# Kernel tuning notes

Measured on AMD Instinct MI355X. Metric: run time of the kernel, lower is better.

Reference implementation:

```python
import jax, jax.numpy as jnp
from jax import lax
import numpy as np

B, TE, TD, C, H, L, V, BLOCK = 2, 1024, 1024, 512, 8, 4, 32000, 1024
HD = C // H  # 64


def setup_inputs() -> dict:
    key = jax.random.key(0)
    ks = iter(jax.random.split(key, 64))
    def w(*shape):
        return jax.random.normal(next(ks), shape, jnp.float32) * 0.02
    d = {}
    d["enc_inp"] = jax.random.randint(next(ks), (B, TE), 0, V, dtype=jnp.int32)
    d["dec_inp"] = jax.random.randint(next(ks), (B, TD), 0, V, dtype=jnp.int32)
    d["enc_inp_mask"] = jnp.ones((B, TE), jnp.int32)
    d["tok_emb"] = w(V, C)
    d["pos_emb"] = w(BLOCK, C)
    for p in ["e", "d_sa", "d_ca"]:
        d[p + "_wq"] = w(L, H, C, HD)
        d[p + "_wk"] = w(L, H, C, HD)
        d[p + "_wv"] = w(L, H, C, HD)
        d[p + "_wo"] = w(L, C, C)
        d[p + "_bo"] = jnp.zeros((L, C), jnp.float32)
    for n in ["e_ln1", "e_ln2", "d_ln1", "d_ln2", "d_ln3"]:
        d[n + "_g"] = jnp.ones((L, C), jnp.float32)
        d[n + "_b"] = jnp.zeros((L, C), jnp.float32)
    for p in ["e", "d"]:
        d[p + "_w1"] = w(L, C, 4 * C)
        d[p + "_b1"] = jnp.zeros((L, 4 * C), jnp.float32)
        d[p + "_w2"] = w(L, 4 * C, C)
        d[p + "_b2"] = jnp.zeros((L, C), jnp.float32)
    d["out_w"] = w(C, V)
    d["out_b"] = jnp.zeros((V,), jnp.float32)
    return d


def _ln(x, g, b):
    m = jnp.mean(x, -1, keepdims=True)
    v = jnp.mean((x - m) ** 2, -1, keepdims=True)
    return (x - m) / jnp.sqrt(v + 1e-5) * g + b


def _mha(x, kv, wq, wk, wv, wo, bo, mask, causal):
    # x: [B,T,C], kv: [B,S,C], wq/wk/wv: [H,C,HD]
    q = jnp.einsum('btc,hcd->bhtd', x, wq)
    k = jnp.einsum('bsc,hcd->bhsd', kv, wk)
    v = jnp.einsum('bsc,hcd->bhsd', kv, wv)
    s = jnp.einsum('bhtd,bhsd->bhts', q, k) * (HD ** -0.5)
    if causal:
        T, S = s.shape[-2], s.shape[-1]
        s = jnp.where(jnp.tril(jnp.ones((T, S), bool)), s, -jnp.inf)
    if mask is not None:
        s = jnp.where(mask[:, None, None, :] != 0, s, -jnp.inf)
    a = jax.nn.softmax(s, axis=-1)
    o = jnp.einsum('bhts,bhsd->bthd', a, v).reshape(x.shape[0], x.shape[1], -1)
    return o @ wo + bo


def reference(enc_inp, dec_inp, enc_inp_mask, tok_emb, pos_emb,
              e_wq, e_wk, e_wv, e_wo, e_bo,
              d_sa_wq, d_sa_wk, d_sa_wv, d_sa_wo, d_sa_bo,
              d_ca_wq, d_ca_wk, d_ca_wv, d_ca_wo, d_ca_bo,
              e_ln1_g, e_ln1_b, e_ln2_g, e_ln2_b,
              d_ln1_g, d_ln1_b, d_ln2_g, d_ln2_b, d_ln3_g, d_ln3_b,
              e_w1, e_b1, e_w2, e_b2, d_w1, d_b1, d_w2, d_b2,
              out_w, out_b):
    enc = tok_emb[enc_inp] + pos_emb[:enc_inp.shape[1]]
    dec = tok_emb[dec_inp] + pos_emb[:dec_inp.shape[1]]

    def enc_step(x, p):
        ln1g, ln1b, wq, wk, wv, wo, bo, ln2g, ln2b, w1, b1, w2, b2 = p
        h = _ln(x, ln1g, ln1b)
        x = x + _mha(h, h, wq, wk, wv, wo, bo, enc_inp_mask, False)
        h = _ln(x, ln2g, ln2b)
        x = x + jnp.maximum(h @ w1 + b1, 0.0) @ w2 + b2
        return x, None

    enc_out, _ = lax.scan(enc_step, enc, (e_ln1_g, e_ln1_b, e_wq, e_wk, e_wv, e_wo, e_bo,
                                          e_ln2_g, e_ln2_b, e_w1, e_b1, e_w2, e_b2))

    def dec_step(x, p):
        (ln1g, ln1b, sawq, sawk, sawv, sawo, sabo,
         ln2g, ln2b, cawq, cawk, cawv, cawo, cabo,
         ln3g, ln3b, w1, b1, w2, b2) = p
        h = _ln(x, ln1g, ln1b)
        x = x + _mha(h, h, sawq, sawk, sawv, sawo, sabo, None, True)
        # torch code applies the same cross-attn LayerNorm to both x and encoder_output
        hq = _ln(x, ln2g, ln2b)
        hk = _ln(enc_out, ln2g, ln2b)
        x = x + _mha(hq, hk, cawq, cawk, cawv, cawo, cabo, enc_inp_mask, False)
        h = _ln(x, ln3g, ln3b)
        x = x + jnp.maximum(h @ w1 + b1, 0.0) @ w2 + b2
        return x, None

    dec_out, _ = lax.scan(dec_step, dec, (d_ln1_g, d_ln1_b, d_sa_wq, d_sa_wk, d_sa_wv, d_sa_wo, d_sa_bo,
                                          d_ln2_g, d_ln2_b, d_ca_wq, d_ca_wk, d_ca_wv, d_ca_wo, d_ca_bo,
                                          d_ln3_g, d_ln3_b, d_w1, d_b1, d_w2, d_b2))

    logits = dec_out @ out_w + out_b  # [B, T_dec, V]
    return logits
```

## Files before the change

### kernel.cpp

```cpp
#include <hip/hip_runtime.h>
#include <hip/hip_bf16.h>
#include <math.h>

#define Cdim 512
#define Hn   8
#define HDim 64
#define Ld   4
#define Tn   1024
#define Bn   2
#define NTOK 2048
#define FF   2048
#define Vn   32000

typedef __bf16 bf16_t;
typedef __bf16 bf16x8 __attribute__((ext_vector_type(8)));
typedef __bf16 bf16x4 __attribute__((ext_vector_type(4)));
typedef float  f32x4  __attribute__((ext_vector_type(4)));

__device__ __forceinline__ void ln_wave(const float* __restrict__ xr,
    const float* __restrict__ g, const float* __restrict__ bb,
    bf16_t* __restrict__ yr, int lane)
{
    f32x4 a = *(const f32x4*)&xr[lane * 8];
    f32x4 c = *(const f32x4*)&xr[lane * 8 + 4];
    float s = a[0] + a[1] + a[2] + a[3] + c[0] + c[1] + c[2] + c[3];
    #pragma unroll
    for (int o = 1; o < 64; o <<= 1) s += __shfl_xor(s, o, 64);
    float mean = s * (1.f / Cdim);
    float d[8], qv = 0.f;
    #pragma unroll
    for (int k = 0; k < 4; k++) { d[k] = a[k] - mean; d[4 + k] = c[k] - mean; }
    #pragma unroll
    for (int k = 0; k < 8; k++) qv += d[k] * d[k];
    #pragma unroll
    for (int o = 1; o < 64; o <<= 1) qv += __shfl_xor(qv, o, 64);
    float inv = rsqrtf(qv * (1.f / Cdim) + 1e-5f);
    f32x4 g0 = *(const f32x4*)&g[lane * 8],  g1 = *(const f32x4*)&g[lane * 8 + 4];
    f32x4 b0 = *(const f32x4*)&bb[lane * 8], b1 = *(const f32x4*)&bb[lane * 8 + 4];
    bf16x8 o;
    #pragma unroll
    for (int k = 0; k < 4; k++) {
        o[k]     = (bf16_t)(d[k]     * inv * g0[k] + b0[k]);
        o[4 + k] = (bf16_t)(d[4 + k] * inv * g1[k] + b1[k]);
    }
    *(bf16x8*)&yr[lane * 8] = o;
}

__global__ __launch_bounds__(256) void ln_k(const float* __restrict__ x,
    const float* __restrict__ g, const float* __restrict__ bb, bf16_t* __restrict__ y)
{
    int wid = threadIdx.x >> 6, lane = threadIdx.x & 63;
    int row = blockIdx.x * 4 + wid;
    ln_wave(x + (long)row * Cdim, g, bb, y + (long)row * Cdim, lane);
}

__global__ __launch_bounds__(256) void ln2_k(const float* __restrict__ x1,
    const float* __restrict__ x2, const float* __restrict__ g,
    const float* __restrict__ bb, bf16_t* __restrict__ y1, bf16_t* __restrict__ y2)
{
    int wid = threadIdx.x >> 6, lane = threadIdx.x & 63;
    int row = blockIdx.x * 4 + wid;
    const float* x = (row < NTOK) ? x1 : x2;
    bf16_t*      y = (row < NTOK) ? y1 : y2;
    int r = row & (NTOK - 1);
    ln_wave(x + (long)r * Cdim, g, bb, y + (long)r * Cdim, lane);
}

__global__ __launch_bounds__(256) void embed_ln_k(const int* __restrict__ inp,
    const float* __restrict__ tok, const float* __restrict__ pos,
    const float* __restrict__ g, const float* __restrict__ bb,
    float* __restrict__ x, bf16_t* __restrict__ y)
{
    int wid = threadIdx.x >> 6, lane = threadIdx.x & 63;
    int bt = blockIdx.x * 4 + wid;
    int t = bt & (Tn - 1);
    long toff = (long)inp[bt] * Cdim;
    f32x4 a = *(const f32x4*)&tok[toff + lane * 8];
    f32x4 c = *(const f32x4*)&tok[toff + lane * 8 + 4];
    f32x4 pa = *(const f32x4*)&pos[(long)t * Cdim + lane * 8];
    f32x4 pc = *(const f32x4*)&pos[(long)t * Cdim + lane * 8 + 4];
    a += pa; c += pc;
    float* xr = x + (long)bt * Cdim;
    *(f32x4*)&xr[lane * 8] = a;
    *(f32x4*)&xr[lane * 8 + 4] = c;
    float s = a[0] + a[1] + a[2] + a[3] + c[0] + c[1] + c[2] + c[3];
    #pragma unroll
    for (int o = 1; o < 64; o <<= 1) s += __shfl_xor(s, o, 64);
    float mean = s * (1.f / Cdim);
    float d[8], qv = 0.f;
    #pragma unroll
    for (int k = 0; k < 4; k++) { d[k] = a[k] - mean; d[4 + k] = c[k] - mean; }
    #pragma unroll
    for (int k = 0; k < 8; k++) qv += d[k] * d[k];
    #pragma unroll
    for (int o = 1; o < 64; o <<= 1) qv += __shfl_xor(qv, o, 64);
    float inv = rsqrtf(qv * (1.f / Cdim) + 1e-5f);
    f32x4 g0 = *(const f32x4*)&g[lane * 8],  g1 = *(const f32x4*)&g[lane * 8 + 4];
    f32x4 b0 = *(const f32x4*)&bb[lane * 8], b1 = *(const f32x4*)&bb[lane * 8 + 4];
    bf16x8 o;
    #pragma unroll
    for (int k = 0; k < 4; k++) {
        o[k]     = (bf16_t)(d[k]     * inv * g0[k] + b0[k]);
        o[4 + k] = (bf16_t)(d[4 + k] * inv * g1[k] + b1[k]);
    }
    *(bf16x8*)&y[(long)bt * Cdim + lane * 8] = o;
}

struct Ptr3 { const float* p[3]; };
__global__ __launch_bounds__(256) void tcvt_b_k(Ptr3 srcs, bf16_t* __restrict__ dst,
    int R, int Cc, int lps, long dstStride)
{
    int z = blockIdx.z; int s = z / lps, l = z - s * lps;
    const float* in = srcs.p[s] + (long)l * R * Cc;
    bf16_t* op = dst + (long)z * dstStride;
    __shared__ float t[64][65];
    int r0 = blockIdx.y * 64, c0 = blockIdx.x * 64;
    int tx = threadIdx.x & 63, ty = threadIdx.x >> 6;
    #pragma unroll
    for (int i = 0; i < 16; i++)
        t[ty + i * 4][tx] = in[(long)(r0 + ty + i * 4) * Cc + c0 + tx];
    __syncthreads();
    #pragma unroll
    for (int i = 0; i < 16; i++) {
        int cc = ty + i * 4;
        op[(long)(c0 + cc) * R + r0 + tx] = (bf16_t)t[tx][cc];
    }
}

struct QkvSrc { const float* p[9]; };
__global__ __launch_bounds__(256) void tcvt_qkv_k(QkvSrc srcs, bf16_t* __restrict__ outp)
{
    int z = blockIdx.z;
    int si = z >> 5, zb = (z >> 3) & 3, zh = z & 7;
    int set = si / 3, part = si - set * 3;
    const float* in = srcs.p[si] + (long)zb * (Hn * Cdim * HDim) + (long)zh * (Cdim * HDim);
    bf16_t* op = outp + ((long)set * Ld + zb) * (1536L * Cdim)
                      + (long)part * 512 * Cdim + (long)zh * 64 * Cdim;
    __shared__ float t[64][65];
    int r0 = blockIdx.y * 64;
    int tx = threadIdx.x & 63, ty = threadIdx.x >> 6;
    #pragma unroll
    for (int i = 0; i < 16; i++)
        t[ty + i * 4][tx] = in[(long)(r0 + ty + i * 4) * HDim + tx];
    __syncthreads();
    #pragma unroll
    for (int i = 0; i < 16; i++) {
        int cc = ty + i * 4;
        op[(long)cc * Cdim + r0 + tx] = (bf16_t)t[tx][cc];
    }
}

template<int BM, int BN, int BK, bool BIAS, bool RELU, bool RES, bool OBF,
         bool VOUT, int SWZM, bool XOUT, bool COAL>
__global__ __launch_bounds__(256) void mgemm_k(
    const bf16_t* __restrict__ A, const bf16_t* __restrict__ A2, int aSplit,
    const bf16_t* __restrict__ Bt, const float* __restrict__ bias,
    const float* __restrict__ res, void* __restrict__ Cout,
    bf16_t* __restrict__ xout, bf16_t* __restrict__ vtout, int vSplit,
    int K, int lda, int ldb, int ldc)
{
    constexpr int MR = BM / 32;
    constexpr int NR = BN / 32;
    constexpr int KK = BK / 32;
    constexpr int LPR = BK / 8;
    __shared__ bf16_t As0[BM * BK];
    __shared__ bf16_t As1[BM * BK];
    __shared__ bf16_t Bs0[BN * BK];
    __shared__ bf16_t Bs1[BN * BK];
    __shared__ float cws[COAL ? 4 * 16 * 36 : 1];

    int tid = threadIdx.x;
    int wv = tid >> 6, lane = tid & 63;
    int bm, bn;
    if constexpr (SWZM > 0) {
        int lin = blockIdx.y * gridDim.x + blockIdx.x;
        int tot = gridDim.x * gridDim.y;
        int chunk = tot >> 3;
        int e = (lin & 7) * chunk + (lin >> 3);
        bm = (e % SWZM) * BM;
        bn = (e / SWZM) * BN;
    } else {
        bm = blockIdx.y * BM; bn = blockIdx.x * BN;
    }
    const bf16_t* Ab = (bn < aSplit) ? A : A2;
    int wr = wv >> 1, wc = wv & 1;

    f32x4 acc[MR][NR];
    #pragma unroll
    for (int i = 0; i < MR; i++)
        #pragma unroll
        for (int j = 0; j < NR; j++)
            acc[i][j] = (f32x4){0.f, 0.f, 0.f, 0.f};

    constexpr int RPW = 512 / BK;
    constexpr int RPP = 2048 / BK;
    const int sr  = lane / LPR;
    const int sc8 = ((lane % LPR) ^ (sr & (LPR - 1))) * 8;
    const int r16 = lane & 15, g4 = lane >> 4;

    auto stage = [&](int k0, bf16_t (&Asb)[BM * BK], bf16_t (&Bsb)[BN * BK]) {
        #pragma unroll
        for (int p = 0; p < BM * BK / 2048; p++) {
            int rb = p * RPP + wv * RPW;
            const bf16_t* g = Ab + (long)(bm + rb + sr) * lda + (k0 + sc8);
            __builtin_amdgcn_global_load_lds(
                (const __attribute__((address_space(1))) void*)g,
                (__attribute__((address_space(3))) void*)&Asb[rb * BK],
                16, 0, 0);
        }
        #pragma unroll
        for (int p = 0; p < BN * BK / 2048; p++) {
            int rb = p * RPP + wv * RPW;
            const bf16_t* g = Bt + (long)(bn + rb + sr) * ldb + (k0 + sc8);
            __builtin_amdgcn_global_load_lds(
                (const __attribute__((address_space(1))) void*)g,
                (__attribute__((address_space(3))) void*)&Bsb[rb * BK],
                16, 0, 0);
        }
    };
    auto compute = [&](bf16_t (&Asb)[BM * BK], bf16_t (&Bsb)[BN * BK]) {
        #pragma unroll
        for (int kk = 0; kk < KK; kk++) {
            bf16x8 bkk[NR];
            #pragma unroll
            for (int j = 0; j < NR; j++) {
                int row = wc * (BN / 2) + j * 16 + r16;
                bkk[j] = *(const bf16x8*)&Bsb[row * BK + (((kk * 4 + g4) ^ (row & (LPR - 1))) * 8)];
            }
            #pragma unroll
            for (int i = 0; i < MR; i++) {
                int row = wr * (BM / 2) + i * 16 + r16;
                bf16x8 a = *(const bf16x8*)&Asb[row * BK + (((kk * 4 + g4) ^ (row & (LPR - 1))) * 8)];
                #pragma unroll
                for (int j = 0; j < NR; j++)
                    acc[i][j] = __builtin_amdgcn_mfma_f32_16x16x32_bf16(a, bkk[j], acc[i][j], 0, 0, 0);
            }
        }
    };

    int nIt = K / BK;
    stage(0, As0, Bs0);
    for (int it = 0; it < nIt; it += 2) {
        __syncthreads();
        if (it + 1 < nIt) stage((it + 1) * BK, As1, Bs1);
        compute(As0, Bs0);
        __syncthreads();
        if (it + 2 < nIt) stage((it + 2) * BK, As0, Bs0);
        if (it + 1 < nIt) compute(As1, Bs1);
    }

    if constexpr (COAL) {
        #pragma unroll
        for (int i = 0; i < MR; i++) {
            int gr0 = bm + wr * (BM / 2) + i * 16;
            #pragma unroll
            for (int hh = 0; hh < NR / 2; hh++) {
                #pragma unroll
                for (int jj = 0; jj < 2; jj++) {
                    int j = hh * 2 + jj;
                    int gc = bn + wc * (BN / 2) + j * 16 + r16;
                    float bv = BIAS ? bias[gc] : 0.f;
                    #pragma unroll
                    for (int q = 0; q < 4; q++) {
                        float v = acc[i][j][q];
                        if (BIAS) v += bv;
                        if (RELU) v = fmaxf(v, 0.f);
                        cws[(wv * 16 + g4 * 4 + q) * 36 + jj * 16 + r16] = v;
                    }
                }
                int gcb = bn + wc * (BN / 2) + hh * 32;
                if constexpr (OBF) {
                    int row = lane >> 2, c8 = (lane & 3) * 8;
                    f32x4 v0 = *(f32x4*)&cws[(wv * 16 + row) * 36 + c8];
                    f32x4 v1 = *(f32x4*)&cws[(wv * 16 + row) * 36 + c8 + 4];
                    long oidx = (long)(gr0 + row) * ldc + gcb + c8;
                    bf16x8 o;
                    #pragma unroll
                    for (int k = 0; k < 4; k++) { o[k] = (bf16_t)v0[k]; o[4 + k] = (bf16_t)v1[k]; }
                    *(bf16x8*)&((bf16_t*)Cout)[oidx] = o;
                } else {
                    #pragma unroll
                    for (int ps = 0; ps < 2; ps++) {
                        int row = (lane >> 3) + 8 * ps, c4 = (lane & 7) * 4;
                        f32x4 v = *(f32x4*)&cws[(wv * 16 + row) * 36 + c4];
                        long oidx = (long)(gr0 + row) * ldc + gcb + c4;
                        if (RES) v += *(const f32x4*)&res[oidx];
                        *(f32x4*)&((float*)Cout)[oidx] = v;
                        if (XOUT) {
                            bf16x4 o;
                            #pragma unroll
                            for (int k = 0; k < 4; k++) o[k] = (bf16_t)v[k];
                            *(bf16x4*)&xout[oidx] = o;
                        }
                    }
                }
            }
        }
    } else {
        #pragma unroll
        for (int i = 0; i < MR; i++) {
            #pragma unroll
            for (int j = 0; j < NR; j++) {
                int gr = bm + wr * (BM / 2) + i * 16 + g4 * 4;
                int gc = bn + wc * (BN / 2) + j * 16 + r16;
                float bv = BIAS ? bias[gc] : 0.f;
                #pragma unroll
                for (int q = 0; q < 4; q++) {
                    float v = acc[i][j][q];
                    if (BIAS) v += bv;
                    if (RELU) v = fmaxf(v, 0.f);
                    if (VOUT && gc >= vSplit) {
                        int row = gr + q;
                        int b = row >> 10, t = row & (Tn - 1);
                        vtout[((long)b * 512 + (gc - vSplit)) * Tn + t] = (bf16_t)v;
                    } else {
                        long oidx = (long)(gr + q) * ldc + gc;
                        if (RES)  v += res[oidx];
                        if (OBF) ((bf16_t*)Cout)[oidx] = (bf16_t)v;
                        else     ((float*) Cout)[oidx] = v;
                        if (XOUT) xout[oidx] = (bf16_t)v;
                    }
                }
            }
        }
    }
}

template<bool CAUSAL, bool HASMASK>
__global__ __launch_bounds__(512, 2) void flash_k(
    const bf16_t* __restrict__ qkv, const bf16_t* __restrict__ vt,
    const int* __restrict__ mask, bf16_t* __restrict__ ao)
{
    __shared__ bf16_t Kl[2][2][64][72];
    __shared__ bf16_t Vl[2][2][64][72];
    __shared__ bf16_t Pl[8][16][72];

    int qt = blockIdx.x, bh = blockIdx.y;
    int b = bh >> 3, h = bh & 7;
    int tid = threadIdx.x, wv = tid >> 6, lane = tid & 63;
    int wg = wv >> 2, wq4 = wv & 3;
    int r16 = lane & 15, g4 = lane >> 4;
    int gtid = tid & 255;

    const bf16_t* qb = qkv + ((long)(b * Tn + qt * 64 + wq4 * 16 + r16)) * 1536 + h * 64;
    bf16x8 aq0 = *(const bf16x8*)&qb[g4 * 8];
    bf16x8 aq1 = *(const bf16x8*)&qb[32 + g4 * 8];

    f32x4 acc[4];
    #pragma unroll
    for (int j = 0; j < 4; j++) acc[j] = (f32x4){0.f, 0.f, 0.f, 0.f};
    float m_[4], l_[4];
    #pragma unroll
    for (int q = 0; q < 4; q++) { m_[q] = -1e30f; l_[q] = 0.f; }

    int lastT = CAUSAL ? qt : (Tn / 64 - 1);
    int niter = CAUSAL ? (qt / 2 + 1) : (Tn / 128);
    int krow = gtid >> 3, kcol = (gtid & 7) * 8;

    bf16x8 kr[2], vr[2];
    int mv = 0;
    {
        int t0 = wg;
        if (t0 <= lastT) {
            int s0 = t0 * 64;
            #pragma unroll
            for (int i = 0; i < 2; i++)
                kr[i] = *(const bf16x8*)&qkv[((long)(b * Tn + s0 + krow + i * 32)) * 1536 + 512 + h * 64 + kcol];
            #pragma unroll
            for (int i = 0; i < 2; i++)
                vr[i] = *(const bf16x8*)&vt[((long)(bh * 64 + krow + i * 32)) * Tn + s0 + kcol];
            if (HASMASK) mv = mask[b * Tn + s0 + lane];
        }
    }

    for (int it = 0; it < niter; it++) {
        int cur = it & 1;
        int t = 2 * it + wg;
        bool active = t <= lastT;
        if (active) {
            #pragma unroll
            for (int i = 0; i < 2; i++) *(bf16x8*)&Kl[cur][wg][krow + i * 32][kcol] = kr[i];
            #pragma unroll
            for (int i = 0; i < 2; i++) *(bf16x8*)&Vl[cur][wg][krow + i * 32][kcol] = vr[i];
        }
        int mv_use = mv;
        __syncthreads();
        int tn = t + 2;
        if (it + 1 < niter && tn <= lastT) {
            int sn = tn * 64;
            #pragma unroll
            for (int i = 0; i < 2; i++)
                kr[i] = *(const bf16x8*)&qkv[((long)(b * Tn + sn + krow + i * 32)) * 1536 + 512 + h * 64 + kcol];
            #pragma unroll
            for (int i = 0; i < 2; i++)
                vr[i] = *(const bf16x8*)&vt[((long)(bh * 64 + krow + i * 32)) * Tn + sn + kcol];
            if (HASMASK) mv = mask[b * Tn + sn + lane];
        }
        if (!active) continue;

        f32x4 scv[4];
        __builtin_amdgcn_s_setprio(1);
        #pragma unroll
        for (int j = 0; j < 4; j++) {
            scv[j] = (f32x4){0.f, 0.f, 0.f, 0.f};
            bf16x8 bk0 = *(const bf16x8*)&Kl[cur][wg][j * 16 + r16][g4 * 8];
            bf16x8 bk1 = *(const bf16x8*)&Kl[cur][wg][j * 16 + r16][32 + g4 * 8];
            scv[j] = __builtin_amdgcn_mfma_f32_16x16x32_bf16(aq0, bk0, scv[j], 0, 0, 0);
            scv[j] = __builtin_amdgcn_mfma_f32_16x16x32_bf16(aq1, bk1, scv[j], 0, 0, 0);
        }
        __builtin_amdgcn_s_setprio(0);

        bool diag = CAUSAL && (t == qt);
        #pragma unroll
        for (int j = 0; j < 4; j++) {
            int col = j * 16 + r16;
            int mm = 1;
            if (HASMASK) mm = __shfl(mv_use, col, 64);
            #pragma unroll
            for (int q = 0; q < 4; q++) {
                float v = scv[j][q] * 0.125f;
                if (diag && col > wq4 * 16 + g4 * 4 + q) v = -1e30f;
                if (HASMASK && mm == 0) v = -1e30f;
                scv[j][q] = v;
            }
        }

        float pmax[4];
        #pragma unroll
        for (int q = 0; q < 4; q++) {
            float v = fmaxf(fmaxf(scv[0][q], scv[1][q]), fmaxf(scv[2][q], scv[3][q]));
            v = fmaxf(v, __shfl_xor(v, 1, 64));
            v = fmaxf(v, __shfl_xor(v, 2, 64));
            v = fmaxf(v, __shfl_xor(v, 4, 64));
            v = fmaxf(v, __shfl_xor(v, 8, 64));
            pmax[q] = v;
        }
        bool skip = __all(pmax[0] <= m_[0] + 8.f && pmax[1] <= m_[1] + 8.f &&
                          pmax[2] <= m_[2] + 8.f && pmax[3] <= m_[3] + 8.f);
        if (!skip) {
            #pragma unroll
            for (int q = 0; q < 4; q++) {
                float mnew = fmaxf(m_[q], pmax[q]);
                float rf = __expf(m_[q] - mnew);
                l_[q] *= rf;
                #pragma unroll
                for (int j = 0; j < 4; j++) acc[j][q] *= rf;
                m_[q] = mnew;
            }
        }
        #pragma unroll
        for (int q = 0; q < 4; q++) {
            float rs = 0.f;
            #pragma unroll
            for (int j = 0; j < 4; j++) {
                float pv = __expf(scv[j][q] - m_[q]);
                scv[j][q] = pv;
                rs += pv;
            }
            rs += __shfl_xor(rs, 1, 64);
            rs += __shfl_xor(rs, 2, 64);
            rs += __shfl_xor(rs, 4, 64);
            rs += __shfl_xor(rs, 8, 64);
            l_[q] += rs;
        }

        #pragma unroll
        for (int j = 0; j < 4; j++)
            #pragma unroll
            for (int q = 0; q < 4; q++)
                Pl[wv][g4 * 4 + q][j * 16 + r16] = (bf16_t)scv[j][q];
        asm volatile("s_waitcnt lgkmcnt(0)" ::: "memory");
        __builtin_amdgcn_sched_barrier(0);

        __builtin_amdgcn_s_setprio(1);
        #pragma unroll
        for (int c = 0; c < 2; c++) {
            bf16x8 pa = *(const bf16x8*)&Pl[wv][r16][c * 32 + g4 * 8];
            #pragma unroll
            for (int j = 0; j < 4; j++) {
                bf16x8 bv = *(const bf16x8*)&Vl[cur][wg][j * 16 + r16][c * 32 + g4 * 8];
                acc[j] = __builtin_amdgcn_mfma_f32_16x16x32_bf16(pa, bv, acc[j], 0, 0, 0);
            }
        }
        __builtin_amdgcn_s_setprio(0);
    }

    float* accS = (float*)&Kl[0][0][0][0];
    float* mlS  = accS + 64 * 64;
    __syncthreads();
    if (wg == 1) {
        #pragma unroll
        for (int j = 0; j < 4; j++)
            #pragma unroll
            for (int q = 0; q < 4; q++)
                accS[(wq4 * 16 + g4 * 4 + q) * 64 + j * 16 + r16] = acc[j][q];
        if (r16 == 0)
            #pragma unroll
            for (int q = 0; q < 4; q++) {
                mlS[(wq4 * 16 + g4 * 4 + q) * 2 + 0] = m_[q];
                mlS[(wq4 * 16 + g4 * 4 + q) * 2 + 1] = l_[q];
            }
    }
    __syncthreads();
    if (wg == 0) {
        bf16_t* aob = ao + ((long)(b * Tn + qt * 64 + wq4 * 16 + g4 * 4)) * Cdim + h * 64;
        #pragma unroll
        for (int q = 0; q < 4; q++) {
            int row = wq4 * 16 + g4 * 4 + q;
            float mB = mlS[row * 2], lB = mlS[row * 2 + 1];
            float mS = fmaxf(m_[q], mB);
            float fA = __expf(m_[q] - mS), fB = __expf(mB - mS);
            float lS = l_[q] * fA + lB * fB;
            float inv = 1.f / lS;
            #pragma unroll
            for (int j = 0; j < 4; j++) {
                float o = (acc[j][q] * fA + accS[row * 64 + j * 16 + r16] * fB) * inv;
                aob[(long)q * Cdim + j * 16 + r16] = (bf16_t)o;
            }
        }
    }
}

static void run_attn(hipStream_t stream, const bf16_t* hq, const bf16_t* hkv,
    const bf16_t* wqkv, const float* bo, const bf16_t* wo_t,
    float* xres, const int* mask, bool causal,
    bf16_t* qkv, bf16_t* vt, bf16_t* ao)
{
    dim3 blk(256);
    mgemm_k<64,128,64,false,false,false,true,true,0,false,false><<<dim3(12, 32, 1), blk, 0, stream>>>(
        hq, hkv, 512, wqkv, nullptr, nullptr, qkv, nullptr, vt, 1024,
        Cdim, Cdim, Cdim, 1536);
    if (causal)
        flash_k<true,false><<<dim3(Tn / 64, Bn * Hn), dim3(512), 0, stream>>>(qkv, vt, nullptr, ao);
    else
        flash_k<false,true><<<dim3(Tn / 64, Bn * Hn), dim3(512), 0, stream>>>(qkv, vt, mask, ao);
    mgemm_k<64,64,64,true,false,true,false,false,0,false,true><<<dim3(8, 32, 1), blk, 0, stream>>>(
        ao, ao, 1 << 30, wo_t, bo, xres, xres, nullptr, nullptr, 1 << 30,
        Cdim, Cdim, Cdim, Cdim);
}

extern "C" void kernel_launch(void* const* d_in, const int* in_sizes, int n_in,
                              void* d_out, int out_size, void* d_ws, size_t ws_size,
                              hipStream_t stream)
{
    (void)in_sizes; (void)n_in; (void)out_size; (void)ws_size;
    const int*   enc_inp  = (const int*)d_in[0];
    const int*   dec_inp  = (const int*)d_in[1];
    const int*   enc_mask = (const int*)d_in[2];
    const float* tok_emb  = (const float*)d_in[3];
    const float* pos_emb  = (const float*)d_in[4];
    const float* e_wq  = (const float*)d_in[5];
    const float* e_wk  = (const float*)d_in[6];
    const float* e_wv  = (const float*)d_in[7];
    const float* e_wo  = (const float*)d_in[8];
    const float* e_bo  = (const float*)d_in[9];
    const float* dsa_wq = (const float*)d_in[10];
    const float* dsa_wk = (const float*)d_in[11];
    const float* dsa_wv = (const float*)d_in[12];
    const float* dsa_wo = (const float*)d_in[13];
    const float* dsa_bo = (const float*)d_in[14];
    const float* dca_wq = (const float*)d_in[15];
    const float* dca_wk = (const float*)d_in[16];
    const float* dca_wv = (const float*)d_in[17];
    const float* dca_wo = (const float*)d_in[18];
    const float* dca_bo = (const float*)d_in[19];
    const float* e_ln1_g = (const float*)d_in[20];
    const float* e_ln1_b = (const float*)d_in[21];
    const float* e_ln2_g = (const float*)d_in[22];
    const float* e_ln2_b = (const float*)d_in[23];
    const float* d_ln1_g = (const float*)d_in[24];
    const float* d_ln1_b = (const float*)d_in[25];
    const float* d_ln2_g = (const float*)d_in[26];
    const float* d_ln2_b = (const float*)d_in[27];
    const float* d_ln3_g = (const float*)d_in[28];
    const float* d_ln3_b = (const float*)d_in[29];
    const float* e_w1 = (const float*)d_in[30];
    const float* e_b1 = (const float*)d_in[31];
    const float* e_w2 = (const float*)d_in[32];
    const float* e_b2 = (const float*)d_in[33];
    const float* d_w1 = (const float*)d_in[34];
    const float* d_b1 = (const float*)d_in[35];
    const float* d_w2 = (const float*)d_in[36];
    const float* d_b2 = (const float*)d_in[37];
    const float* out_w = (const float*)d_in[38];
    const float* out_b = (const float*)d_in[39];
    float* out = (float*)d_out;

    char* p = (char*)d_ws;
    auto takeB = [&](size_t bytes) { char* r = p; p += (bytes + 255) & ~(size_t)255; return r; };
    float*  x_enc = (float*)takeB(1048576ull * 4);
    float*  x_dec = (float*)takeB(1048576ull * 4);
    bf16_t* h     = (bf16_t*)takeB(1048576ull * 2);
    bf16_t* hk    = (bf16_t*)takeB(1048576ull * 2);
    bf16_t* qkv   = (bf16_t*)takeB(3145728ull * 2);
    bf16_t* vt    = (bf16_t*)takeB(1048576ull * 2);
    bf16_t* ao    = (bf16_t*)takeB(1048576ull * 2);
    bf16_t* xdb   = (bf16_t*)takeB(1048576ull * 2);
    bf16_t* mid   = (bf16_t*)takeB(4194304ull * 2);
    bf16_t* wqkv_t = (bf16_t*)takeB(12ull * 786432 * 2);
    bf16_t* wo_t   = (bf16_t*)takeB(12ull * 262144 * 2);
    bf16_t* w1_t   = (bf16_t*)takeB(8ull * 1048576 * 2);
    bf16_t* w2_t   = (bf16_t*)takeB(8ull * 1048576 * 2);
    bf16_t* outw_t = (bf16_t*)takeB(16384000ull * 2);

    dim3 blk(256);
    const long LQKV = 1536L * Cdim;

    QkvSrc qs;
    qs.p[0] = e_wq;   qs.p[1] = e_wk;   qs.p[2] = e_wv;
    qs.p[3] = dsa_wq; qs.p[4] = dsa_wk; qs.p[5] = dsa_wv;
    qs.p[6] = dca_wq; qs.p[7] = dca_wk; qs.p[8] = dca_wv;
    tcvt_qkv_k<<<dim3(1, 8, 288), blk, 0, stream>>>(qs, wqkv_t);
    Ptr3 pw;
    pw.p[0] = e_wo; pw.p[1] = dsa_wo; pw.p[2] = dca_wo;
    tcvt_b_k<<<dim3(8, 8, 12), blk, 0, stream>>>(pw, wo_t, Cdim, Cdim, 4, (long)Cdim * Cdim);
    pw.p[0] = e_w1; pw.p[1] = d_w1; pw.p[2] = nullptr;
    tcvt_b_k<<<dim3(32, 8, 8), blk, 0, stream>>>(pw, w1_t, Cdim, FF, 4, (long)Cdim * FF);
    pw.p[0] = e_w2; pw.p[1] = d_w2; pw.p[2] = nullptr;
    tcvt_b_k<<<dim3(8, 32, 8), blk, 0, stream>>>(pw, w2_t, FF, Cdim, 4, (long)FF * Cdim);
    pw.p[0] = out_w; pw.p[1] = nullptr; pw.p[2] = nullptr;
    tcvt_b_k<<<dim3(500, 8, 1), blk, 0, stream>>>(pw, outw_t, Cdim, Vn, 1, 0);

    embed_ln_k<<<NTOK / 4, blk, 0, stream>>>(enc_inp, tok_emb, pos_emb, e_ln1_g, e_ln1_b, x_enc, h);
    for (int l = 0; l < Ld; l++) {
        if (l) ln_k<<<NTOK / 4, blk, 0, stream>>>(x_enc, e_ln1_g + l * Cdim, e_ln1_b + l * Cdim, h);
        run_attn(stream, h, h,
                 wqkv_t + (long)l * LQKV, e_bo + l * Cdim, wo_t + (long)l * Cdim * Cdim,
                 x_enc, enc_mask, false, qkv, vt, ao);
        ln_k<<<NTOK / 4, blk, 0, stream>>>(x_enc, e_ln2_g + l * Cdim, e_ln2_b + l * Cdim, h);
        mgemm_k<128,128,64,true,true,false,true,false,0,false,true><<<dim3(16, 16, 1), blk, 0, stream>>>(
            h, h, 1 << 30, w1_t + (long)l * Cdim * FF, e_b1 + l * FF, nullptr, mid,
            nullptr, nullptr, 1 << 30, Cdim, Cdim, Cdim, FF);
        mgemm_k<64,64,64,true,false,true,false,false,0,false,true><<<dim3(8, 32, 1), blk, 0, stream>>>(
            mid, mid, 1 << 30, w2_t + (long)l * FF * Cdim, e_b2 + l * Cdim, x_enc, x_enc,
            nullptr, nullptr, 1 << 30, FF, FF, FF, Cdim);
    }

    embed_ln_k<<<NTOK / 4, blk, 0, stream>>>(dec_inp, tok_emb, pos_emb, d_ln1_g, d_ln1_b, x_dec, h);
    for (int l = 0; l < Ld; l++) {
        if (l) ln_k<<<NTOK / 4, blk, 0, stream>>>(x_dec, d_ln1_g + l * Cdim, d_ln1_b + l * Cdim, h);
        run_attn(stream, h, h,
                 wqkv_t + (long)(Ld + l) * LQKV, dsa_bo + l * Cdim,
                 wo_t + (long)(Ld + l) * Cdim * Cdim,
                 x_dec, nullptr, true, qkv, vt, ao);
        ln2_k<<<2 * NTOK / 4, blk, 0, stream>>>(x_dec, x_enc,
            d_ln2_g + l * Cdim, d_ln2_b + l * Cdim, h, hk);
        run_attn(stream, h, hk,
                 wqkv_t + (long)(2 * Ld + l) * LQKV, dca_bo + l * Cdim,
                 wo_t + (long)(2 * Ld + l) * Cdim * Cdim,
                 x_dec, enc_mask, false, qkv, vt, ao);
        ln_k<<<NTOK / 4, blk, 0, stream>>>(x_dec, d_ln3_g + l * Cdim, d_ln3_b + l * Cdim, h);
        mgemm_k<128,128,64,true,true,false,true,false,0,false,true><<<dim3(16, 16, 1), blk, 0, stream>>>(
            h, h, 1 << 30, w1_t + (long)(Ld + l) * Cdim * FF, d_b1 + l * FF, nullptr, mid,
            nullptr, nullptr, 1 << 30, Cdim, Cdim, Cdim, FF);
        if (l < Ld - 1)
            mgemm_k<64,64,64,true,false,true,false,false,0,false,true><<<dim3(8, 32, 1), blk, 0, stream>>>(
                mid, mid, 1 << 30, w2_t + (long)(Ld + l) * FF * Cdim, d_b2 + l * Cdim, x_dec, x_dec,
                nullptr, nullptr, 1 << 30, FF, FF, FF, Cdim);
        else
            mgemm_k<64,64,64,true,false,true,false,false,0,true,true><<<dim3(8, 32, 1), blk, 0, stream>>>(
                mid, mid, 1 << 30, w2_t + (long)(Ld + l) * FF * Cdim, d_b2 + l * Cdim, x_dec, x_dec,
                xdb, nullptr, 1 << 30, FF, FF, FF, Cdim);
    }

    mgemm_k<128,128,64,true,false,false,false,false,16,false,true><<<dim3(250, 16, 1), blk, 0, stream>>>(
        xdb, xdb, 1 << 30, outw_t, out_b, nullptr, out, nullptr, nullptr, 1 << 30,
        Cdim, Cdim, Cdim, Vn);
}
```

Before: 1.005 ms.

## Fuse LayerNorm into GEMM A-operand loading and merge embedding kernels

```diff
diff --git a/kernel.cpp b/kernel.cpp
--- a/kernel.cpp
+++ b/kernel.cpp
@@ -17,93 +17,23 @@
 typedef __bf16 bf16x4 __attribute__((ext_vector_type(4)));
 typedef float  f32x4  __attribute__((ext_vector_type(4)));
 
-__device__ __forceinline__ void ln_wave(const float* __restrict__ xr,
-    const float* __restrict__ g, const float* __restrict__ bb,
-    bf16_t* __restrict__ yr, int lane)
-{
-    f32x4 a = *(const f32x4*)&xr[lane * 8];
-    f32x4 c = *(const f32x4*)&xr[lane * 8 + 4];
-    float s = a[0] + a[1] + a[2] + a[3] + c[0] + c[1] + c[2] + c[3];
-    #pragma unroll
-    for (int o = 1; o < 64; o <<= 1) s += __shfl_xor(s, o, 64);
-    float mean = s * (1.f / Cdim);
-    float d[8], qv = 0.f;
-    #pragma unroll
-    for (int k = 0; k < 4; k++) { d[k] = a[k] - mean; d[4 + k] = c[k] - mean; }
-    #pragma unroll
-    for (int k = 0; k < 8; k++) qv += d[k] * d[k];
-    #pragma unroll
-    for (int o = 1; o < 64; o <<= 1) qv += __shfl_xor(qv, o, 64);
-    float inv = rsqrtf(qv * (1.f / Cdim) + 1e-5f);
-    f32x4 g0 = *(const f32x4*)&g[lane * 8],  g1 = *(const f32x4*)&g[lane * 8 + 4];
-    f32x4 b0 = *(const f32x4*)&bb[lane * 8], b1 = *(const f32x4*)&bb[lane * 8 + 4];
-    bf16x8 o;
-    #pragma unroll
-    for (int k = 0; k < 4; k++) {
-        o[k]     = (bf16_t)(d[k]     * inv * g0[k] + b0[k]);
-        o[4 + k] = (bf16_t)(d[4 + k] * inv * g1[k] + b1[k]);
-    }
-    *(bf16x8*)&yr[lane * 8] = o;
-}
-
-__global__ __launch_bounds__(256) void ln_k(const float* __restrict__ x,
-    const float* __restrict__ g, const float* __restrict__ bb, bf16_t* __restrict__ y)
+__global__ __launch_bounds__(256) void embed2_k(const int* __restrict__ enc_inp,
+    const int* __restrict__ dec_inp, const float* __restrict__ tok,
+    const float* __restrict__ pos, float* __restrict__ x_enc, float* __restrict__ x_dec)
 {
     int wid = threadIdx.x >> 6, lane = threadIdx.x & 63;
     int row = blockIdx.x * 4 + wid;
-    ln_wave(x + (long)row * Cdim, g, bb, y + (long)row * Cdim, lane);
-}
-
-__global__ __launch_bounds__(256) void ln2_k(const float* __restrict__ x1,
-    const float* __restrict__ x2, const float* __restrict__ g,
-    const float* __restrict__ bb, bf16_t* __restrict__ y1, bf16_t* __restrict__ y2)
-{
-    int wid = threadIdx.x >> 6, lane = threadIdx.x & 63;
-    int row = blockIdx.x * 4 + wid;
-    const float* x = (row < NTOK) ? x1 : x2;
-    bf16_t*      y = (row < NTOK) ? y1 : y2;
-    int r = row & (NTOK - 1);
-    ln_wave(x + (long)r * Cdim, g, bb, y + (long)r * Cdim, lane);
-}
-
-__global__ __launch_bounds__(256) void embed_ln_k(const int* __restrict__ inp,
-    const float* __restrict__ tok, const float* __restrict__ pos,
-    const float* __restrict__ g, const float* __restrict__ bb,
-    float* __restrict__ x, bf16_t* __restrict__ y)
-{
-    int wid = threadIdx.x >> 6, lane = threadIdx.x & 63;
-    int bt = blockIdx.x * 4 + wid;
+    const int* inp = (row < NTOK) ? enc_inp : dec_inp;
+    float* x       = (row < NTOK) ? x_enc   : x_dec;
+    int bt = row & (NTOK - 1);
     int t = bt & (Tn - 1);
     long toff = (long)inp[bt] * Cdim;
     f32x4 a = *(const f32x4*)&tok[toff + lane * 8];
     f32x4 c = *(const f32x4*)&tok[toff + lane * 8 + 4];
-    f32x4 pa = *(const f32x4*)&pos[(long)t * Cdim + lane * 8];
-    f32x4 pc = *(const f32x4*)&pos[(long)t * Cdim + lane * 8 + 4];
-    a += pa; c += pc;
-    float* xr = x + (long)bt * Cdim;
-    *(f32x4*)&xr[lane * 8] = a;
-    *(f32x4*)&xr[lane * 8 + 4] = c;
-    float s = a[0] + a[1] + a[2] + a[3] + c[0] + c[1] + c[2] + c[3];
-    #pragma unroll
-    for (int o = 1; o < 64; o <<= 1) s += __shfl_xor(s, o, 64);
-    float mean = s * (1.f / Cdim);
-    float d[8], qv = 0.f;
-    #pragma unroll
-    for (int k = 0; k < 4; k++) { d[k] = a[k] - mean; d[4 + k] = c[k] - mean; }
-    #pragma unroll
-    for (int k = 0; k < 8; k++) qv += d[k] * d[k];
-    #pragma unroll
-    for (int o = 1; o < 64; o <<= 1) qv += __shfl_xor(qv, o, 64);
-    float inv = rsqrtf(qv * (1.f / Cdim) + 1e-5f);
-    f32x4 g0 = *(const f32x4*)&g[lane * 8],  g1 = *(const f32x4*)&g[lane * 8 + 4];
-    f32x4 b0 = *(const f32x4*)&bb[lane * 8], b1 = *(const f32x4*)&bb[lane * 8 + 4];
-    bf16x8 o;
-    #pragma unroll
-    for (int k = 0; k < 4; k++) {
-        o[k]     = (bf16_t)(d[k]     * inv * g0[k] + b0[k]);
-        o[4 + k] = (bf16_t)(d[4 + k] * inv * g1[k] + b1[k]);
-    }
-    *(bf16x8*)&y[(long)bt * Cdim + lane * 8] = o;
+    a += *(const f32x4*)&pos[(long)t * Cdim + lane * 8];
+    c += *(const f32x4*)&pos[(long)t * Cdim + lane * 8 + 4];
+    *(f32x4*)&x[(long)bt * Cdim + lane * 8] = a;
+    *(f32x4*)&x[(long)bt * Cdim + lane * 8 + 4] = c;
 }
 
 struct Ptr3 { const float* p[3]; };
@@ -150,10 +80,11 @@
     }
 }
 
-template<int BM, int BN, int BK, bool BIAS, bool RELU, bool RES, bool OBF,
+template<int BM, int BN, int BK, bool ALN, bool BIAS, bool RELU, bool RES, bool OBF,
          bool VOUT, int SWZM, bool XOUT, bool COAL>
 __global__ __launch_bounds__(256) void mgemm_k(
-    const bf16_t* __restrict__ A, const bf16_t* __restrict__ A2, int aSplit,
+    const void* __restrict__ Av, const void* __restrict__ A2v, int aSplit,
+    const float* __restrict__ gamma, const float* __restrict__ beta,
     const bf16_t* __restrict__ Bt, const float* __restrict__ bias,
     const float* __restrict__ res, void* __restrict__ Cout,
     bf16_t* __restrict__ xout, bf16_t* __restrict__ vtout, int vSplit,
@@ -168,6 +99,8 @@
     __shared__ bf16_t Bs0[BN * BK];
     __shared__ bf16_t Bs1[BN * BK];
     __shared__ float cws[COAL ? 4 * 16 * 36 : 1];
+    __shared__ float mS[ALN ? BM : 1];
+    __shared__ float rS[ALN ? BM : 1];
 
     int tid = threadIdx.x;
     int wv = tid >> 6, lane = tid & 63;
@@ -182,7 +115,7 @@
     } else {
         bm = blockIdx.y * BM; bn = blockIdx.x * BN;
     }
-    const bf16_t* Ab = (bn < aSplit) ? A : A2;
+    const void* Abv = (bn < aSplit) ? Av : A2v;
     int wr = wv >> 1, wc = wv & 1;
 
     f32x4 acc[MR][NR];
@@ -198,7 +131,32 @@
     const int sc8 = ((lane % LPR) ^ (sr & (LPR - 1))) * 8;
     const int r16 = lane & 15, g4 = lane >> 4;
 
-    auto stage = [&](int k0, bf16_t (&Asb)[BM * BK], bf16_t (&Bsb)[BN * BK]) {
+    const float* Af = (const float*)Abv;
+    if constexpr (ALN) {
+        constexpr int TPR = 256 / BM;
+        int rowI = tid / TPR, sub = tid % TPR;
+        int cpt = K / TPR;
+        const float* rp = Af + (long)(bm + rowI) * lda + sub * cpt;
+        float s = 0.f, s2 = 0.f;
+        for (int c = 0; c < cpt; c += 4) {
+            f32x4 v = *(const f32x4*)&rp[c];
+            s  += v[0] + v[1] + v[2] + v[3];
+            s2 += v[0]*v[0] + v[1]*v[1] + v[2]*v[2] + v[3]*v[3];
+        }
+        s  += __shfl_xor(s, 1, 64);  s2 += __shfl_xor(s2, 1, 64);
+        if (TPR == 4) { s += __shfl_xor(s, 2, 64); s2 += __shfl_xor(s2, 2, 64); }
+        if (sub == 0) {
+            float invK = 1.f / (float)K;
+            float mu = s * invK;
+            float var = s2 * invK - mu * mu;
+            mS[rowI] = mu;
+            rS[rowI] = rsqrtf(var + 1e-5f);
+        }
+        __syncthreads();
+    }
+
+    auto stageA = [&](int k0, bf16_t (&Asb)[BM * BK]) {
+        const bf16_t* Ab = (const bf16_t*)Abv;
         #pragma unroll
         for (int p = 0; p < BM * BK / 2048; p++) {
             int rb = p * RPP + wv * RPW;
@@ -208,6 +166,8 @@
                 (__attribute__((address_space(3))) void*)&Asb[rb * BK],
                 16, 0, 0);
         }
+    };
+    auto stageB = [&](int k0, bf16_t (&Bsb)[BN * BK]) {
         #pragma unroll
         for (int p = 0; p < BN * BK / 2048; p++) {
             int rb = p * RPP + wv * RPW;
@@ -218,6 +178,33 @@
                 16, 0, 0);
         }
     };
+    const int aRow = tid >> 3, aCI = tid & 7;
+    auto aload = [&](int k0, f32x4 (&ar)[BM / 32][2]) {
+        #pragma unroll
+        for (int p = 0; p < BM / 32; p++) {
+            const float* g = Af + (long)(bm + p * 32 + aRow) * lda + k0 + aCI * 8;
+            ar[p][0] = *(const f32x4*)g;
+            ar[p][1] = *(const f32x4*)(g + 4);
+        }
+    };
+    auto awrite = [&](bf16_t (&Asb)[BM * BK], f32x4 (&ar)[BM / 32][2], int k0) {
+        f32x4 gm0 = *(const f32x4*)&gamma[k0 + aCI * 8];
+        f32x4 gm1 = *(const f32x4*)&gamma[k0 + aCI * 8 + 4];
+        f32x4 bt0 = *(const f32x4*)&beta[k0 + aCI * 8];
+        f32x4 bt1 = *(const f32x4*)&beta[k0 + aCI * 8 + 4];
+        #pragma unroll
+        for (int p = 0; p < BM / 32; p++) {
+            int row = p * 32 + aRow;
+            float mu = mS[row], rs = rS[row];
+            bf16x8 o;
+            #pragma unroll
+            for (int k = 0; k < 4; k++) {
+                o[k]     = (bf16_t)((ar[p][0][k] - mu) * rs * gm0[k] + bt0[k]);
+                o[4 + k] = (bf16_t)((ar[p][1][k] - mu) * rs * gm1[k] + bt1[k]);
+            }
+            *(bf16x8*)&Asb[row * BK + ((aCI ^ (row & 7)) * 8)] = o;
+        }
+    };
     auto compute = [&](bf16_t (&Asb)[BM * BK], bf16_t (&Bsb)[BN * BK]) {
         #pragma unroll
         for (int kk = 0; kk < KK; kk++) {
@@ -239,14 +226,30 @@
     };
 
     int nIt = K / BK;
-    stage(0, As0, Bs0);
-    for (int it = 0; it < nIt; it += 2) {
+    if constexpr (ALN) {
+        f32x4 ar[BM / 32][2];
+        aload(0, ar); stageB(0, Bs0); awrite(As0, ar, 0);
         __syncthreads();
-        if (it + 1 < nIt) stage((it + 1) * BK, As1, Bs1);
-        compute(As0, Bs0);
-        __syncthreads();
-        if (it + 2 < nIt) stage((it + 2) * BK, As0, Bs0);
-        if (it + 1 < nIt) compute(As1, Bs1);
+        for (int it = 0; it < nIt; it += 2) {
+            if (it + 1 < nIt) { aload((it + 1) * BK, ar); stageB((it + 1) * BK, Bs1); }
+            compute(As0, Bs0);
+            if (it + 1 < nIt) awrite(As1, ar, (it + 1) * BK);
+            __syncthreads();
+            if (it + 2 < nIt) { aload((it + 2) * BK, ar); stageB((it + 2) * BK, Bs0); }
+            if (it + 1 < nIt) compute(As1, Bs1);
+            if (it + 2 < nIt) awrite(As0, ar, (it + 2) * BK);
+            __syncthreads();
+        }
+    } else {
+        stageA(0, As0); stageB(0, Bs0);
+        for (int it = 0; it < nIt; it += 2) {
+            __syncthreads();
+            if (it + 1 < nIt) { stageA((it + 1) * BK, As1); stageB((it + 1) * BK, Bs1); }
+            compute(As0, Bs0);
+            __syncthreads();
+            if (it + 2 < nIt) { stageA((it + 2) * BK, As0); stageB((it + 2) * BK, Bs0); }
+            if (it + 1 < nIt) compute(As1, Bs1);
+        }
     }
 
     if constexpr (COAL) {
@@ -508,8 +511,8 @@
         for (int q = 0; q < 4; q++) {
             int row = wq4 * 16 + g4 * 4 + q;
             float mB = mlS[row * 2], lB = mlS[row * 2 + 1];
-            float mS = fmaxf(m_[q], mB);
-            float fA = __expf(m_[q] - mS), fB = __expf(mB - mS);
+            float mS2 = fmaxf(m_[q], mB);
+            float fA = __expf(m_[q] - mS2), fB = __expf(mB - mS2);
             float lS = l_[q] * fA + lB * fB;
             float inv = 1.f / lS;
             #pragma unroll
@@ -521,21 +524,22 @@
     }
 }
 
-static void run_attn(hipStream_t stream, const bf16_t* hq, const bf16_t* hkv,
+static void run_attn(hipStream_t stream, const float* xq, const float* xkv,
+    const float* lng, const float* lnb,
     const bf16_t* wqkv, const float* bo, const bf16_t* wo_t,
     float* xres, const int* mask, bool causal,
     bf16_t* qkv, bf16_t* vt, bf16_t* ao)
 {
     dim3 blk(256);
-    mgemm_k<64,128,64,false,false,false,true,true,0,false,false><<<dim3(12, 32, 1), blk, 0, stream>>>(
-        hq, hkv, 512, wqkv, nullptr, nullptr, qkv, nullptr, vt, 1024,
+    mgemm_k<64,128,64,true,false,false,false,true,true,0,false,false><<<dim3(12, 32, 1), blk, 0, stream>>>(
+        xq, xkv, 512, lng, lnb, wqkv, nullptr, nullptr, qkv, nullptr, vt, 1024,
         Cdim, Cdim, Cdim, 1536);
     if (causal)
         flash_k<true,false><<<dim3(Tn / 64, Bn * Hn), dim3(512), 0, stream>>>(qkv, vt, nullptr, ao);
     else
         flash_k<false,true><<<dim3(Tn / 64, Bn * Hn), dim3(512), 0, stream>>>(qkv, vt, mask, ao);
-    mgemm_k<64,64,64,true,false,true,false,false,0,false,true><<<dim3(8, 32, 1), blk, 0, stream>>>(
-        ao, ao, 1 << 30, wo_t, bo, xres, xres, nullptr, nullptr, 1 << 30,
+    mgemm_k<64,64,64,false,true,false,true,false,false,0,false,true><<<dim3(8, 32, 1), blk, 0, stream>>>(
+        ao, ao, 1 << 30, nullptr, nullptr, wo_t, bo, xres, xres, nullptr, nullptr, 1 << 30,
         Cdim, Cdim, Cdim, Cdim);
 }
 
@@ -590,8 +594,6 @@
     auto takeB = [&](size_t bytes) { char* r = p; p += (bytes + 255) & ~(size_t)255; return r; };
     float*  x_enc = (float*)takeB(1048576ull * 4);
     float*  x_dec = (float*)takeB(1048576ull * 4);
-    bf16_t* h     = (bf16_t*)takeB(1048576ull * 2);
-    bf16_t* hk    = (bf16_t*)takeB(1048576ull * 2);
     bf16_t* qkv   = (bf16_t*)takeB(3145728ull * 2);
     bf16_t* vt    = (bf16_t*)takeB(1048576ull * 2);
     bf16_t* ao    = (bf16_t*)takeB(1048576ull * 2);
@@ -621,49 +623,45 @@
     pw.p[0] = out_w; pw.p[1] = nullptr; pw.p[2] = nullptr;
     tcvt_b_k<<<dim3(500, 8, 1), blk, 0, stream>>>(pw, outw_t, Cdim, Vn, 1, 0);
 
-    embed_ln_k<<<NTOK / 4, blk, 0, stream>>>(enc_inp, tok_emb, pos_emb, e_ln1_g, e_ln1_b, x_enc, h);
+    embed2_k<<<2 * NTOK / 4, blk, 0, stream>>>(enc_inp, dec_inp, tok_emb, pos_emb, x_enc, x_dec);
+
     for (int l = 0; l < Ld; l++) {
-        if (l) ln_k<<<NTOK / 4, blk, 0, stream>>>(x_enc, e_ln1_g + l * Cdim, e_ln1_b + l * Cdim, h);
-        run_attn(stream, h, h,
+        run_attn(stream, x_enc, x_enc, e_ln1_g + l * Cdim, e_ln1_b + l * Cdim,
                  wqkv_t + (long)l * LQKV, e_bo + l * Cdim, wo_t + (long)l * Cdim * Cdim,
                  x_enc, enc_mask, false, qkv, vt, ao);
-        ln_k<<<NTOK / 4, blk, 0, stream>>>(x_enc, e_ln2_g + l * Cdim, e_ln2_b + l * Cdim, h);
-        mgemm_k<128,128,64,true,true,false,true,false,0,false,true><<<dim3(16, 16, 1), blk, 0, stream>>>(
-            h, h, 1 << 30, w1_t + (long)l * Cdim * FF, e_b1 + l * FF, nullptr, mid,
+        mgemm_k<128,128,64,true,true,true,false,true,false,0,false,true><<<dim3(16, 16, 1), blk, 0, stream>>>(
+            x_enc, x_enc, 1 << 30, e_ln2_g + l * Cdim, e_ln2_b + l * Cdim,
+            w1_t + (long)l * Cdim * FF, e_b1 + l * FF, nullptr, mid,
             nullptr, nullptr, 1 << 30, Cdim, Cdim, Cdim, FF);
-        mgemm_k<64,64,64,true,false,true,false,false,0,false,true><<<dim3(8, 32, 1), blk, 0, stream>>>(
-            mid, mid, 1 << 30, w2_t + (long)l * FF * Cdim, e_b2 + l * Cdim, x_enc, x_enc,
-            nullptr, nullptr, 1 << 30, FF, FF, FF, Cdim);
-    }
-
-    embed_ln_k<<<NTOK / 4, blk, 0, stream>>>(dec_inp, tok_emb, pos_emb, d_ln1_g, d_ln1_b, x_dec, h);
+        mgemm_k<64,64,64,false,true,false,true,false,false,0,false,true><<<dim3(8, 32, 1), blk, 0, stream>>>(
+            mid, mid, 1 << 30, nullptr, nullptr, w2_t + (long)l * FF * Cdim, e_b2 + l * Cdim,
+            x_enc, x_enc, nullptr, nullptr, 1 << 30, FF, FF, FF, Cdim);
+    }
+
     for (int l = 0; l < Ld; l++) {
-        if (l) ln_k<<<NTOK / 4, blk, 0, stream>>>(x_dec, d_ln1_g + l * Cdim, d_ln1_b + l * Cdim, h);
-        run_attn(stream, h, h,
+        run_attn(stream, x_dec, x_dec, d_ln1_g + l * Cdim, d_ln1_b + l * Cdim,
                  wqkv_t + (long)(Ld + l) * LQKV, dsa_bo + l * Cdim,
                  wo_t + (long)(Ld + l) * Cdim * Cdim,
                  x_dec, nullptr, true, qkv, vt, ao);
-        ln2_k<<<2 * NTOK / 4, blk, 0, stream>>>(x_dec, x_enc,
-            d_ln2_g + l * Cdim, d_ln2_b + l * Cdim, h, hk);
-        run_attn(stream, h, hk,
+        run_attn(stream, x_dec, x_enc, d_ln2_g + l * Cdim, d_ln2_b + l * Cdim,
                  wqkv_t + (long)(2 * Ld + l) * LQKV, dca_bo + l * Cdim,
                  wo_t + (long)(2 * Ld + l) * Cdim * Cdim,
                  x_dec, enc_mask, false, qkv, vt, ao);
-        ln_k<<<NTOK / 4, blk, 0, stream>>>(x_dec, d_ln3_g + l * Cdim, d_ln3_b + l * Cdim, h);
-        mgemm_k<128,128,64,true,true,false,true,false,0,false,true><<<dim3(16, 16, 1), blk, 0, stream>>>(
-            h, h, 1 << 30, w1_t + (long)(Ld + l) * Cdim * FF, d_b1 + l * FF, nullptr, mid,
+        mgemm_k<128,128,64,true,true,true,false,true,false,0,false,true><<<dim3(16, 16, 1), blk, 0, stream>>>(
+            x_dec, x_dec, 1 << 30, d_ln3_g + l * Cdim, d_ln3_b + l * Cdim,
+            w1_t + (long)(Ld + l) * Cdim * FF, d_b1 + l * FF, nullptr, mid,
             nullptr, nullptr, 1 << 30, Cdim, Cdim, Cdim, FF);
         if (l < Ld - 1)
-            mgemm_k<64,64,64,true,false,true,false,false,0,false,true><<<dim3(8, 32, 1), blk, 0, stream>>>(
-                mid, mid, 1 << 30, w2_t + (long)(Ld + l) * FF * Cdim, d_b2 + l * Cdim, x_dec, x_dec,
-                nullptr, nullptr, 1 << 30, FF, FF, FF, Cdim);
+            mgemm_k<64,64,64,false,true,false,true,false,false,0,false,true><<<dim3(8, 32, 1), blk, 0, stream>>>(
+                mid, mid, 1 << 30, nullptr, nullptr, w2_t + (long)(Ld + l) * FF * Cdim, d_b2 + l * Cdim,
+                x_dec, x_dec, nullptr, nullptr, 1 << 30, FF, FF, FF, Cdim);
         else
-            mgemm_k<64,64,64,true,false,true,false,false,0,true,true><<<dim3(8, 32, 1), blk, 0, stream>>>(
-                mid, mid, 1 << 30, w2_t + (long)(Ld + l) * FF * Cdim, d_b2 + l * Cdim, x_dec, x_dec,
-                xdb, nullptr, 1 << 30, FF, FF, FF, Cdim);
-    }
-
-    mgemm_k<128,128,64,true,false,false,false,false,16,false,true><<<dim3(250, 16, 1), blk, 0, stream>>>(
-        xdb, xdb, 1 << 30, outw_t, out_b, nullptr, out, nullptr, nullptr, 1 << 30,
+            mgemm_k<64,64,64,false,true,false,true,false,false,0,true,true><<<dim3(8, 32, 1), blk, 0, stream>>>(
+                mid, mid, 1 << 30, nullptr, nullptr, w2_t + (long)(Ld + l) * FF * Cdim, d_b2 + l * Cdim,
+                x_dec, x_dec, xdb, nullptr, 1 << 30, FF, FF, FF, Cdim);
+    }
+
+    mgemm_k<128,128,64,false,true,false,false,false,false,16,false,true><<<dim3(250, 16, 1), blk, 0, stream>>>(
+        xdb, xdb, 1 << 30, nullptr, nullptr, outw_t, out_b, nullptr, out, nullptr, nullptr, 1 << 30,
         Cdim, Cdim, Cdim, Vn);
 }
```

Result: slower. 1.258 ms (+25.2%).
